# Kernel optimization log

Hardware: AMD Instinct MI355X
Metric: run time of the kernel (lower is better)

The kernel has to match this reference:

```python
import jax, jax.numpy as jnp
import numpy as np

NUM_HEADS = 16
PAD_ID = 0.0  # max(config.pad_id, 0)


def setup_inputs() -> dict:
    key = jax.random.key(0)
    ks = jax.random.split(key, 9)
    B, T, C = 2, 2048, 1024
    x = jax.random.normal(ks[0], (B, T, C), dtype=jnp.float32)
    # xavier_uniform-like scale for square [C, C] weights
    lim = (6.0 / (C + C)) ** 0.5
    def w(k):
        return jax.random.uniform(k, (C, C), dtype=jnp.float32, minval=-lim, maxval=lim)
    def b(k):
        return jax.random.uniform(k, (C,), dtype=jnp.float32)  # nn.init.uniform_ default [0,1)
    return {
        "x": x,
        "wq_w": w(ks[1]), "wq_b": b(ks[2]),
        "wk_w": w(ks[3]), "wk_b": b(ks[4]),
        "wv_w": w(ks[5]), "wv_b": b(ks[6]),
        "wo_w": w(ks[7]), "wo_b": b(ks[8]),
    }


def reference(x, wq_w, wq_b, wk_w, wk_b, wv_w, wv_b, wo_w, wo_b):
    B, T, C = x.shape
    H = NUM_HEADS
    Dh = C // H
    scale = Dh ** -0.5

    # Linear layers (torch Linear: x @ W.T + b), then split heads -> [B, T, H, Dh]
    q = (x @ wq_w.T + wq_b).reshape(B, T, H, Dh)
    k = (x @ wk_w.T + wk_b).reshape(B, T, H, Dh)
    v = (x @ wv_w.T + wv_b).reshape(B, T, H, Dh)

    # scores: [B, H, Tq, Tk]
    scores = jnp.einsum("bthd,bshd->bhts", q, k) * scale

    # Padding mask over keys: (x[:,:,0] != pad_id) -> [B, 1, 1, Tk]
    key_mask = (x[:, :, 0] != PAD_ID)[:, None, None, :]
    scores = jnp.where(key_mask, scores, -jnp.inf)

    attn = jax.nn.softmax(scores, axis=-1)

    out = jnp.einsum("bhts,bshd->bthd", attn, v).reshape(B, T, C)
    return out @ wo_w.T + wo_b
```

## Files before the change

### kernel.cpp

```cpp
#include <hip/hip_runtime.h>
#include <hip/hip_bf16.h>

typedef short short8 __attribute__((ext_vector_type(8)));
typedef float f32x4 __attribute__((ext_vector_type(4)));

#define MFMA32(a, b, c) __builtin_amdgcn_mfma_f32_16x16x32_bf16(a, b, c, 0, 0, 0)

#if __has_builtin(__builtin_amdgcn_exp2f)
#define EXP2F(x) __builtin_amdgcn_exp2f(x)
#else
#define EXP2F(x) exp2f(x)
#endif

#define GLL16(gp, lp) __builtin_amdgcn_global_load_lds(                                  \
    (__attribute__((address_space(1))) unsigned int*)(unsigned long long)(const void*)(gp), \
    (__attribute__((address_space(3))) unsigned int*)(lp), 16, 0, 0)

__device__ __forceinline__ unsigned short f2b(float f) {
    union { float f; unsigned int u; } v;
    v.f = f;
    unsigned int u = v.u;
    return (unsigned short)((u + 0x7fffu + ((u >> 16) & 1u)) >> 16);
}

static __device__ __forceinline__ f32x4 max4(f32x4 x, f32x4 y) {
    f32x4 r;
    r[0] = fmaxf(x[0], y[0]); r[1] = fmaxf(x[1], y[1]);
    r[2] = fmaxf(x[2], y[2]); r[3] = fmaxf(x[3], y[3]);
    return r;
}

__global__ void cvt_all(const float* __restrict__ x,
                        const float* __restrict__ w0, const float* __restrict__ w1,
                        const float* __restrict__ w2, const float* __restrict__ w3,
                        unsigned short* __restrict__ xb, unsigned short* __restrict__ wb,
                        float* __restrict__ maskbuf) {
    int blk = blockIdx.x;
    if (blk < 4096) {
        int i = blk * 256 + threadIdx.x;
        float4 v = ((const float4*)x)[i];
        ushort4 o;
        o.x = f2b(v.x); o.y = f2b(v.y); o.z = f2b(v.z); o.w = f2b(v.w);
        ((ushort4*)xb)[i] = o;
        if ((i & 255) == 0)
            maskbuf[i >> 8] = (v.x != 0.0f) ? 0.0f : -1e30f;
    } else {
        int wi = blk - 4096;
        int widx = wi >> 10;
        int i = (wi & 1023) * 256 + threadIdx.x;
        const float* src = widx == 0 ? w0 : (widx == 1 ? w1 : (widx == 2 ? w2 : w3));
        float4 v = ((const float4*)src)[i];
        ushort4 o;
        o.x = f2b(v.x); o.y = f2b(v.y); o.z = f2b(v.z); o.w = f2b(v.w);
        ((ushort4*)(wb + ((size_t)widx << 20)))[i] = o;
    }
}

#define QSCALE (0.125f * 1.44269504088896341f)

__global__ __launch_bounds__(256) void gemm_qkv(
        const unsigned short* __restrict__ A,
        const unsigned short* __restrict__ wq, const unsigned short* __restrict__ wk,
        const unsigned short* __restrict__ wv,
        const float* __restrict__ bq, const float* __restrict__ bk,
        const float* __restrict__ bv,
        unsigned short* __restrict__ qbuf, unsigned short* __restrict__ kbuf,
        unsigned short* __restrict__ vbuf) {
    __shared__ __attribute__((aligned(16))) unsigned short As[2][128 * 32];
    __shared__ __attribute__((aligned(16))) unsigned short Bs[2][128 * 32];
    int tid = threadIdx.x;
    int lane = tid & 63, wave = tid >> 6;
    int lane15 = lane & 15, quad = lane >> 4;
    int seg = blockIdx.x >> 3;
    int bn = (blockIdx.x & 7) * 128;
    int bm = blockIdx.y * 128;
    const unsigned short* Bw = seg == 0 ? wq : (seg == 1 ? wk : wv);
    const float* bias = seg == 0 ? bq : (seg == 1 ? bk : bv);
    int wm = (wave >> 1) * 64, wn = (wave & 1) * 64;

    f32x4 acc[4][4];
#pragma unroll
    for (int i = 0; i < 4; i++)
#pragma unroll
        for (int j = 0; j < 4; j++) acc[i][j] = (f32x4){0.f, 0.f, 0.f, 0.f};

    int arow = tid >> 2, acol = (tid & 3) * 8;
    const unsigned short* A0 = &A[(size_t)(bm + arow) * 1024 + acol];
    const unsigned short* A1 = A0 + (size_t)64 * 1024;
    const unsigned short* B0 = &Bw[(size_t)(bn + arow) * 1024 + acol];
    const unsigned short* B1 = B0 + (size_t)64 * 1024;

    GLL16(A0, &As[0][(size_t)tid * 8]);
    GLL16(A1, &As[0][(size_t)(tid + 256) * 8]);
    GLL16(B0, &Bs[0][(size_t)tid * 8]);
    GLL16(B1, &Bs[0][(size_t)(tid + 256) * 8]);

    for (int it = 0; it < 32; it++) {
        int cur = it & 1;
        __syncthreads();
        if (it < 31) {
            int kn = (it + 1) * 32;
            GLL16(A0 + kn, &As[cur ^ 1][(size_t)tid * 8]);
            GLL16(A1 + kn, &As[cur ^ 1][(size_t)(tid + 256) * 8]);
            GLL16(B0 + kn, &Bs[cur ^ 1][(size_t)tid * 8]);
            GLL16(B1 + kn, &Bs[cur ^ 1][(size_t)(tid + 256) * 8]);
        }
        const unsigned short* as = As[cur];
        const unsigned short* bs = Bs[cur];
        short8 af[4], bf[4];
#pragma unroll
        for (int i = 0; i < 4; i++)
            af[i] = *(const short8*)&as[(wm + i * 16 + lane15) * 32 + quad * 8];
#pragma unroll
        for (int j = 0; j < 4; j++)
            bf[j] = *(const short8*)&bs[(wn + j * 16 + lane15) * 32 + quad * 8];
#pragma unroll
        for (int i = 0; i < 4; i++)
#pragma unroll
            for (int j = 0; j < 4; j++)
                acc[i][j] = MFMA32(af[i], bf[j], acc[i][j]);
    }

    int bb = bm >> 11;
#pragma unroll
    for (int j = 0; j < 4; j++) {
        int nl = bn + wn + j * 16 + lane15;
        int h = nl >> 6, d = nl & 63;
        float bv_ = bias[nl];
        if (seg == 2) {
            size_t vbase = ((size_t)((bb * 16 + h) * 64 + d)) * 2048;
#pragma unroll
            for (int i = 0; i < 4; i++) {
                int tk0 = (bm & 2047) + wm + i * 16 + quad * 4;
                int grp = tk0 >> 5;
                ushort4 pk;
                pk.x = f2b(acc[i][j][0] + bv_);
                pk.y = f2b(acc[i][j][1] + bv_);
                pk.z = f2b(acc[i][j][2] + bv_);
                pk.w = f2b(acc[i][j][3] + bv_);
                *(ushort4*)&vbuf[vbase + grp * 32 + quad * 8 + (i & 1) * 4] = pk;
            }
        } else {
#pragma unroll
            for (int i = 0; i < 4; i++)
#pragma unroll
                for (int r = 0; r < 4; r++) {
                    int m = bm + wm + i * 16 + quad * 4 + r;
                    int tk = m & 2047;
                    float v = acc[i][j][r] + bv_;
                    size_t off = ((size_t)((bb * 16 + h) * 2048 + tk)) * 64 + d;
                    if (seg == 0) qbuf[off] = f2b(v * QSCALE);
                    else          kbuf[off] = f2b(v);
                }
        }
    }
}

__global__ __launch_bounds__(256) void gemm_proj(
        const unsigned short* __restrict__ A, const unsigned short* __restrict__ Bw,
        const float* __restrict__ bias, float* __restrict__ out) {
    __shared__ __attribute__((aligned(16))) unsigned short As[2][64 * 32];
    __shared__ __attribute__((aligned(16))) unsigned short Bs[2][128 * 32];
    int tid = threadIdx.x;
    int lane = tid & 63, wave = tid >> 6;
    int lane15 = lane & 15, quad = lane >> 4;
    int bn = blockIdx.x * 128, bm = blockIdx.y * 64;
    int wm = (wave >> 1) * 32, wn = (wave & 1) * 64;

    f32x4 acc[2][4];
#pragma unroll
    for (int i = 0; i < 2; i++)
#pragma unroll
        for (int j = 0; j < 4; j++) acc[i][j] = (f32x4){0.f, 0.f, 0.f, 0.f};

    int arow = tid >> 2, acol = (tid & 3) * 8;
    const unsigned short* A0 = &A[(size_t)(bm + arow) * 1024 + acol];
    const unsigned short* B0 = &Bw[(size_t)(bn + arow) * 1024 + acol];
    const unsigned short* B1 = B0 + (size_t)64 * 1024;

    GLL16(A0, &As[0][(size_t)tid * 8]);
    GLL16(B0, &Bs[0][(size_t)tid * 8]);
    GLL16(B1, &Bs[0][(size_t)(tid + 256) * 8]);

    for (int it = 0; it < 32; it++) {
        int cur = it & 1;
        __syncthreads();
        if (it < 31) {
            int kn = (it + 1) * 32;
            GLL16(A0 + kn, &As[cur ^ 1][(size_t)tid * 8]);
            GLL16(B0 + kn, &Bs[cur ^ 1][(size_t)tid * 8]);
            GLL16(B1 + kn, &Bs[cur ^ 1][(size_t)(tid + 256) * 8]);
        }
        const unsigned short* as = As[cur];
        const unsigned short* bs = Bs[cur];
        short8 af[2], bf[4];
#pragma unroll
        for (int i = 0; i < 2; i++)
            af[i] = *(const short8*)&as[(wm + i * 16 + lane15) * 32 + quad * 8];
#pragma unroll
        for (int j = 0; j < 4; j++)
            bf[j] = *(const short8*)&bs[(wn + j * 16 + lane15) * 32 + quad * 8];
#pragma unroll
        for (int i = 0; i < 2; i++)
#pragma unroll
            for (int j = 0; j < 4; j++)
                acc[i][j] = MFMA32(af[i], bf[j], acc[i][j]);
    }

#pragma unroll
    for (int j = 0; j < 4; j++) {
        int n = bn + wn + j * 16 + lane15;
        float bv_ = bias[n];
#pragma unroll
        for (int i = 0; i < 2; i++)
#pragma unroll
            for (int r = 0; r < 4; r++) {
                int m = bm + wm + i * 16 + quad * 4 + r;
                out[(size_t)m * 1024 + n] = acc[i][j][r] + bv_;
            }
    }
}

__global__ __launch_bounds__(256, 2) void attn_kernel(
        const unsigned short* __restrict__ qbuf, const unsigned short* __restrict__ kbuf,
        const unsigned short* __restrict__ vtbuf, const float* __restrict__ maskbuf,
        unsigned short* __restrict__ attnout) {
    __shared__ __attribute__((aligned(16))) unsigned short Ks[2][128 * 64];
    __shared__ __attribute__((aligned(16))) unsigned short Vs[2][64 * 128];

    int id = blockIdx.x;
    int combo = (id & 7) | (((id >> 7) & 3) << 3);
    int qt = (id >> 3) & 15;
    int b = combo >> 4, h = combo & 15;
    int tid = threadIdx.x, lane = tid & 63, wave = tid >> 6;
    int lane15 = lane & 15, quad = lane >> 4;
    int q0 = qt * 128 + wave * 32;

    const unsigned short* Q  = qbuf  + (size_t)combo * 2048 * 64;
    const unsigned short* Kp = kbuf  + (size_t)combo * 2048 * 64;
    const unsigned short* Vt = vtbuf + (size_t)combo * 64 * 2048;
    const float* mb = maskbuf + b * 2048;

    short8 qf[2][2];
#pragma unroll
    for (int a = 0; a < 2; a++)
#pragma unroll
        for (int g = 0; g < 2; g++)
            qf[a][g] = *(const short8*)&Q[(size_t)(q0 + a * 16 + lane15) * 64 + g * 32 + quad * 8];

    int ci0 = tid;
    float m_run[2] = {-1e30f, -1e30f}, l_run[2] = {0.f, 0.f};
    f32x4 o[2][4];
#pragma unroll
    for (int a = 0; a < 2; a++)
#pragma unroll
        for (int c = 0; c < 4; c++) o[a][c] = (f32x4){0.f, 0.f, 0.f, 0.f};

    const f32x4 z4 = {0.f, 0.f, 0.f, 0.f};
    int x7 = lane15 & 7;

#pragma unroll
    for (int r4 = 0; r4 < 4; r4++) {
        int ci = ci0 + r4 * 256;
        int kr = ci >> 3, kc = (ci & 7) ^ (kr & 7);
        GLL16(&Kp[(size_t)kr * 64 + kc * 8], &Ks[0][(size_t)ci * 8]);
        int vd = ci >> 4, vc = (ci & 15) ^ (vd & 15);
        GLL16(&Vt[(size_t)vd * 2048 + vc * 8], &Vs[0][(size_t)ci * 8]);
    }

    for (int it = 0; it < 16; it++) {
        int cur = it & 1;
        int kb = it * 128;
        __syncthreads();
        if (it < 15) {
            int kn = kb + 128;
#pragma unroll
            for (int r4 = 0; r4 < 4; r4++) {
                int ci = ci0 + r4 * 256;
                int kr = ci >> 3, kc = (ci & 7) ^ (kr & 7);
                GLL16(&Kp[(size_t)(kn + kr) * 64 + kc * 8], &Ks[cur ^ 1][(size_t)ci * 8]);
                int vd = ci >> 4, vc = (ci & 15) ^ (vd & 15);
                GLL16(&Vt[(size_t)vd * 2048 + kn + vc * 8], &Vs[cur ^ 1][(size_t)ci * 8]);
            }
        }
        const unsigned short* ks = Ks[cur];
        const unsigned short* vs = Vs[cur];

        f32x4 s[2][8];
#pragma unroll
        for (int t = 0; t < 8; t++) {
            int row = t * 16 + lane15;
            short8 k0 = *(const short8*)&ks[row * 64 + (quad ^ x7) * 8];
            short8 k1 = *(const short8*)&ks[row * 64 + ((quad + 4) ^ x7) * 8];
            f32x4 t0 = MFMA32(k0, qf[0][0], z4);
            s[0][t] = MFMA32(k1, qf[0][1], t0);
            f32x4 t1 = MFMA32(k0, qf[1][0], z4);
            s[1][t] = MFMA32(k1, qf[1][1], t1);
        }
#pragma unroll
        for (int t = 0; t < 8; t++) {
            f32x4 mkt = *(const f32x4*)&mb[kb + t * 16 + quad * 4];
            s[0][t] += mkt;
            s[1][t] += mkt;
        }
        short8 pb8[2][4];
#pragma unroll
        for (int a = 0; a < 2; a++) {
            f32x4 m4 = s[a][0];
#pragma unroll
            for (int t = 1; t < 8; t++) m4 = max4(m4, s[a][t]);
            float mx = fmaxf(fmaxf(m4[0], m4[1]), fmaxf(m4[2], m4[3]));
            mx = fmaxf(mx, __shfl_xor(mx, 16));
            mx = fmaxf(mx, __shfl_xor(mx, 32));
            float mnew = fmaxf(m_run[a], mx);
            float alpha = EXP2F(m_run[a] - mnew);
            m_run[a] = mnew;
            float ls = 0.f;
#pragma unroll
            for (int g = 0; g < 4; g++) {
                float e0 = EXP2F(s[a][2 * g][0] - mnew);
                float e1 = EXP2F(s[a][2 * g][1] - mnew);
                float e2 = EXP2F(s[a][2 * g][2] - mnew);
                float e3 = EXP2F(s[a][2 * g][3] - mnew);
                float f0 = EXP2F(s[a][2 * g + 1][0] - mnew);
                float f1 = EXP2F(s[a][2 * g + 1][1] - mnew);
                float f2 = EXP2F(s[a][2 * g + 1][2] - mnew);
                float f3 = EXP2F(s[a][2 * g + 1][3] - mnew);
                ls += ((e0 + e1) + (e2 + e3)) + ((f0 + f1) + (f2 + f3));
                union { uint4 u; short8 sv; } pu;
                pu.u.x = __builtin_amdgcn_perm(__float_as_uint(e1), __float_as_uint(e0), 0x07060302u);
                pu.u.y = __builtin_amdgcn_perm(__float_as_uint(e3), __float_as_uint(e2), 0x07060302u);
                pu.u.z = __builtin_amdgcn_perm(__float_as_uint(f1), __float_as_uint(f0), 0x07060302u);
                pu.u.w = __builtin_amdgcn_perm(__float_as_uint(f3), __float_as_uint(f2), 0x07060302u);
                pb8[a][g] = pu.sv;
            }
            l_run[a] = l_run[a] * alpha + ls;
#pragma unroll
            for (int c = 0; c < 4; c++) o[a][c] *= alpha;
        }
#pragma unroll
        for (int c = 0; c < 4; c++) {
            int d = c * 16 + lane15;
#pragma unroll
            for (int g = 0; g < 4; g++) {
                int skc = (g * 4 + quad) ^ lane15;
                short8 vv = *(const short8*)&vs[d * 128 + skc * 8];
                o[0][c] = MFMA32(vv, pb8[0][g], o[0][c]);
                o[1][c] = MFMA32(vv, pb8[1][g], o[1][c]);
            }
        }
    }

#pragma unroll
    for (int a = 0; a < 2; a++) {
        float l = l_run[a];
        l += __shfl_xor(l, 16);
        l += __shfl_xor(l, 32);
        float rl = 1.0f / l;
        size_t row = (size_t)(b * 2048 + q0 + a * 16 + lane15) * 1024 + h * 64 + quad * 4;
#pragma unroll
        for (int c = 0; c < 4; c++) {
            ushort4 pk;
            pk.x = f2b(o[a][c][0] * rl);
            pk.y = f2b(o[a][c][1] * rl);
            pk.z = f2b(o[a][c][2] * rl);
            pk.w = f2b(o[a][c][3] * rl);
            *(ushort4*)&attnout[row + c * 16] = pk;
        }
    }
}

extern "C" void kernel_launch(void* const* d_in, const int* in_sizes, int n_in,
                              void* d_out, int out_size, void* d_ws, size_t ws_size,
                              hipStream_t stream) {
    const float* x    = (const float*)d_in[0];
    const float* wq_w = (const float*)d_in[1];
    const float* wq_b = (const float*)d_in[2];
    const float* wk_w = (const float*)d_in[3];
    const float* wk_b = (const float*)d_in[4];
    const float* wv_w = (const float*)d_in[5];
    const float* wv_b = (const float*)d_in[6];
    const float* wo_w = (const float*)d_in[7];
    const float* wo_b = (const float*)d_in[8];
    float* out = (float*)d_out;

    char* ws = (char*)d_ws;
    size_t off = 0;
    unsigned short* xb      = (unsigned short*)(ws + off); off += (size_t)4096 * 1024 * 2;
    unsigned short* wb      = (unsigned short*)(ws + off); off += (size_t)4 * 1024 * 1024 * 2;
    unsigned short* qbuf    = (unsigned short*)(ws + off); off += (size_t)4096 * 1024 * 2;
    unsigned short* kbuf    = (unsigned short*)(ws + off); off += (size_t)4096 * 1024 * 2;
    unsigned short* vbuf    = (unsigned short*)(ws + off); off += (size_t)4096 * 1024 * 2;
    unsigned short* attnout = (unsigned short*)(ws + off); off += (size_t)4096 * 1024 * 2;
    float* maskbuf          = (float*)(ws + off);          off += 4096 * 4;

    unsigned short* wqb = wb;
    unsigned short* wkb = wb + (1u << 20);
    unsigned short* wvb = wb + (2u << 20);
    unsigned short* wob = wb + (3u << 20);

    cvt_all<<<8192, 256, 0, stream>>>(x, wq_w, wk_w, wv_w, wo_w, xb, wb, maskbuf);

    gemm_qkv<<<dim3(24, 32), 256, 0, stream>>>(xb, wqb, wkb, wvb,
                                               wq_b, wk_b, wv_b, qbuf, kbuf, vbuf);

    attn_kernel<<<512, 256, 0, stream>>>(qbuf, kbuf, vbuf, maskbuf, attnout);

    gemm_proj<<<dim3(8, 64), 256, 0, stream>>>(attnout, wob, wo_b, out);
}
```

Before: 218.5 us.

## Load K/V fragments directly from global into registers, dropping LDS double buffer

The attention kernel no longer stages K and V tiles through double-buffered shared memory with global_load_lds and __syncthreads. Each wave now loads its own K and V MFMA fragments straight from global memory into registers, prefetching V while the softmax runs. It also raises wave priority around the MFMA sections with s_setprio. This removes block-level barriers and LDS traffic, but every wave in the block re-reads the same K/V tiles from global/L2 instead of sharing them, and register pressure rises.

```diff
diff --git a/kernel.cpp b/kernel.cpp
--- a/kernel.cpp
+++ b/kernel.cpp
@@ -225,9 +225,6 @@
         const unsigned short* __restrict__ qbuf, const unsigned short* __restrict__ kbuf,
         const unsigned short* __restrict__ vtbuf, const float* __restrict__ maskbuf,
         unsigned short* __restrict__ attnout) {
-    __shared__ __attribute__((aligned(16))) unsigned short Ks[2][128 * 64];
-    __shared__ __attribute__((aligned(16))) unsigned short Vs[2][64 * 128];
-
     int id = blockIdx.x;
     int combo = (id & 7) | (((id >> 7) & 3) << 3);
     int qt = (id >> 3) & 15;
@@ -248,7 +245,6 @@
         for (int g = 0; g < 2; g++)
             qf[a][g] = *(const short8*)&Q[(size_t)(q0 + a * 16 + lane15) * 64 + g * 32 + quad * 8];
 
-    int ci0 = tid;
     float m_run[2] = {-1e30f, -1e30f}, l_run[2] = {0.f, 0.f};
     f32x4 o[2][4];
 #pragma unroll
@@ -257,52 +253,46 @@
         for (int c = 0; c < 4; c++) o[a][c] = (f32x4){0.f, 0.f, 0.f, 0.f};
 
     const f32x4 z4 = {0.f, 0.f, 0.f, 0.f};
-    int x7 = lane15 & 7;
-
-#pragma unroll
-    for (int r4 = 0; r4 < 4; r4++) {
-        int ci = ci0 + r4 * 256;
-        int kr = ci >> 3, kc = (ci & 7) ^ (kr & 7);
-        GLL16(&Kp[(size_t)kr * 64 + kc * 8], &Ks[0][(size_t)ci * 8]);
-        int vd = ci >> 4, vc = (ci & 15) ^ (vd & 15);
-        GLL16(&Vt[(size_t)vd * 2048 + vc * 8], &Vs[0][(size_t)ci * 8]);
-    }
+
+    const unsigned short* Krow = &Kp[(size_t)lane15 * 64 + quad * 8];
+    const unsigned short* Vrow = &Vt[(size_t)lane15 * 2048 + quad * 8];
 
     for (int it = 0; it < 16; it++) {
-        int cur = it & 1;
         int kb = it * 128;
-        __syncthreads();
-        if (it < 15) {
-            int kn = kb + 128;
-#pragma unroll
-            for (int r4 = 0; r4 < 4; r4++) {
-                int ci = ci0 + r4 * 256;
-                int kr = ci >> 3, kc = (ci & 7) ^ (kr & 7);
-                GLL16(&Kp[(size_t)(kn + kr) * 64 + kc * 8], &Ks[cur ^ 1][(size_t)ci * 8]);
-                int vd = ci >> 4, vc = (ci & 15) ^ (vd & 15);
-                GLL16(&Vt[(size_t)vd * 2048 + kn + vc * 8], &Vs[cur ^ 1][(size_t)ci * 8]);
-            }
-        }
-        const unsigned short* ks = Ks[cur];
-        const unsigned short* vs = Vs[cur];
+
+        short8 k0[8], k1[8];
+#pragma unroll
+        for (int t = 0; t < 8; t++) {
+            const unsigned short* kr = Krow + (size_t)(kb + t * 16) * 64;
+            k0[t] = *(const short8*)kr;
+            k1[t] = *(const short8*)(kr + 32);
+        }
 
         f32x4 s[2][8];
+        __builtin_amdgcn_s_setprio(1);
 #pragma unroll
         for (int t = 0; t < 8; t++) {
-            int row = t * 16 + lane15;
-            short8 k0 = *(const short8*)&ks[row * 64 + (quad ^ x7) * 8];
-            short8 k1 = *(const short8*)&ks[row * 64 + ((quad + 4) ^ x7) * 8];
-            f32x4 t0 = MFMA32(k0, qf[0][0], z4);
-            s[0][t] = MFMA32(k1, qf[0][1], t0);
-            f32x4 t1 = MFMA32(k0, qf[1][0], z4);
-            s[1][t] = MFMA32(k1, qf[1][1], t1);
-        }
+            f32x4 t0 = MFMA32(k0[t], qf[0][0], z4);
+            s[0][t] = MFMA32(k1[t], qf[0][1], t0);
+            f32x4 t1 = MFMA32(k0[t], qf[1][0], z4);
+            s[1][t] = MFMA32(k1[t], qf[1][1], t1);
+        }
+        __builtin_amdgcn_s_setprio(0);
+
+        short8 vf[4][4];
+#pragma unroll
+        for (int c = 0; c < 4; c++)
+#pragma unroll
+            for (int g = 0; g < 4; g++)
+                vf[c][g] = *(const short8*)(Vrow + (size_t)c * 16 * 2048 + kb + g * 32);
+
 #pragma unroll
         for (int t = 0; t < 8; t++) {
             f32x4 mkt = *(const f32x4*)&mb[kb + t * 16 + quad * 4];
             s[0][t] += mkt;
             s[1][t] += mkt;
         }
+
         short8 pb8[2][4];
 #pragma unroll
         for (int a = 0; a < 2; a++) {
@@ -338,17 +328,16 @@
 #pragma unroll
             for (int c = 0; c < 4; c++) o[a][c] *= alpha;
         }
-#pragma unroll
-        for (int c = 0; c < 4; c++) {
-            int d = c * 16 + lane15;
+
+        __builtin_amdgcn_s_setprio(1);
+#pragma unroll
+        for (int c = 0; c < 4; c++)
 #pragma unroll
             for (int g = 0; g < 4; g++) {
-                int skc = (g * 4 + quad) ^ lane15;
-                short8 vv = *(const short8*)&vs[d * 128 + skc * 8];
-                o[0][c] = MFMA32(vv, pb8[0][g], o[0][c]);
-                o[1][c] = MFMA32(vv, pb8[1][g], o[1][c]);
+                o[0][c] = MFMA32(vf[c][g], pb8[0][g], o[0][c]);
+                o[1][c] = MFMA32(vf[c][g], pb8[1][g], o[1][c]);
             }
-        }
+        __builtin_amdgcn_s_setprio(0);
     }
 
 #pragma unroll
```

Measured after the change: 273.1 us. 25.0% more time.

## Split attention block into 8 waves of 16 query rows each

Applied to the files above, without the earlier changes.

The attention kernel now launches 512 threads per block, and each of the 8 waves handles 16 query rows instead of 32. This halves per-wave register state (Q fragments, score tiles, accumulators), allows more waves per CU via launch bounds (512,4), and spreads the K/V tile load across more threads. In exchange, every K and V fragment read from LDS now feeds only one MFMA instead of two, so LDS traffic per FLOP doubles and there is less instruction-level parallelism per wave.

```diff
diff --git a/kernel.cpp b/kernel.cpp
--- a/kernel.cpp
+++ b/kernel.cpp
@@ -221,7 +221,7 @@
     }
 }
 
-__global__ __launch_bounds__(256, 2) void attn_kernel(
+__global__ __launch_bounds__(512, 4) void attn_kernel(
         const unsigned short* __restrict__ qbuf, const unsigned short* __restrict__ kbuf,
         const unsigned short* __restrict__ vtbuf, const float* __restrict__ maskbuf,
         unsigned short* __restrict__ attnout) {
@@ -234,34 +234,30 @@
     int b = combo >> 4, h = combo & 15;
     int tid = threadIdx.x, lane = tid & 63, wave = tid >> 6;
     int lane15 = lane & 15, quad = lane >> 4;
-    int q0 = qt * 128 + wave * 32;
+    int q0 = qt * 128 + wave * 16;
 
     const unsigned short* Q  = qbuf  + (size_t)combo * 2048 * 64;
     const unsigned short* Kp = kbuf  + (size_t)combo * 2048 * 64;
     const unsigned short* Vt = vtbuf + (size_t)combo * 64 * 2048;
     const float* mb = maskbuf + b * 2048;
 
-    short8 qf[2][2];
-#pragma unroll
-    for (int a = 0; a < 2; a++)
-#pragma unroll
-        for (int g = 0; g < 2; g++)
-            qf[a][g] = *(const short8*)&Q[(size_t)(q0 + a * 16 + lane15) * 64 + g * 32 + quad * 8];
-
-    int ci0 = tid;
-    float m_run[2] = {-1e30f, -1e30f}, l_run[2] = {0.f, 0.f};
-    f32x4 o[2][4];
-#pragma unroll
-    for (int a = 0; a < 2; a++)
-#pragma unroll
-        for (int c = 0; c < 4; c++) o[a][c] = (f32x4){0.f, 0.f, 0.f, 0.f};
+    short8 qf[2];
+#pragma unroll
+    for (int g = 0; g < 2; g++)
+        qf[g] = *(const short8*)&Q[(size_t)(q0 + lane15) * 64 + g * 32 + quad * 8];
+
+    float m_run = -1e30f, l_run = 0.f;
+    f32x4 o[4];
+#pragma unroll
+    for (int c = 0; c < 4; c++) o[c] = (f32x4){0.f, 0.f, 0.f, 0.f};
 
     const f32x4 z4 = {0.f, 0.f, 0.f, 0.f};
     int x7 = lane15 & 7;
-
-#pragma unroll
-    for (int r4 = 0; r4 < 4; r4++) {
-        int ci = ci0 + r4 * 256;
+    int ci0 = tid;
+
+#pragma unroll
+    for (int r2 = 0; r2 < 2; r2++) {
+        int ci = ci0 + r2 * 512;
         int kr = ci >> 3, kc = (ci & 7) ^ (kr & 7);
         GLL16(&Kp[(size_t)kr * 64 + kc * 8], &Ks[0][(size_t)ci * 8]);
         int vd = ci >> 4, vc = (ci & 15) ^ (vd & 15);
@@ -275,8 +271,8 @@
         if (it < 15) {
             int kn = kb + 128;
 #pragma unroll
-            for (int r4 = 0; r4 < 4; r4++) {
-                int ci = ci0 + r4 * 256;
+            for (int r2 = 0; r2 < 2; r2++) {
+                int ci = ci0 + r2 * 512;
                 int kr = ci >> 3, kc = (ci & 7) ^ (kr & 7);
                 GLL16(&Kp[(size_t)(kn + kr) * 64 + kc * 8], &Ks[cur ^ 1][(size_t)ci * 8]);
                 int vd = ci >> 4, vc = (ci & 15) ^ (vd & 15);
@@ -286,58 +282,52 @@
         const unsigned short* ks = Ks[cur];
         const unsigned short* vs = Vs[cur];
 
-        f32x4 s[2][8];
+        f32x4 s[8];
 #pragma unroll
         for (int t = 0; t < 8; t++) {
             int row = t * 16 + lane15;
             short8 k0 = *(const short8*)&ks[row * 64 + (quad ^ x7) * 8];
             short8 k1 = *(const short8*)&ks[row * 64 + ((quad + 4) ^ x7) * 8];
-            f32x4 t0 = MFMA32(k0, qf[0][0], z4);
-            s[0][t] = MFMA32(k1, qf[0][1], t0);
-            f32x4 t1 = MFMA32(k0, qf[1][0], z4);
-            s[1][t] = MFMA32(k1, qf[1][1], t1);
-        }
-#pragma unroll
-        for (int t = 0; t < 8; t++) {
-            f32x4 mkt = *(const f32x4*)&mb[kb + t * 16 + quad * 4];
-            s[0][t] += mkt;
-            s[1][t] += mkt;
-        }
-        short8 pb8[2][4];
-#pragma unroll
-        for (int a = 0; a < 2; a++) {
-            f32x4 m4 = s[a][0];
-#pragma unroll
-            for (int t = 1; t < 8; t++) m4 = max4(m4, s[a][t]);
-            float mx = fmaxf(fmaxf(m4[0], m4[1]), fmaxf(m4[2], m4[3]));
-            mx = fmaxf(mx, __shfl_xor(mx, 16));
-            mx = fmaxf(mx, __shfl_xor(mx, 32));
-            float mnew = fmaxf(m_run[a], mx);
-            float alpha = EXP2F(m_run[a] - mnew);
-            m_run[a] = mnew;
-            float ls = 0.f;
-#pragma unroll
-            for (int g = 0; g < 4; g++) {
-                float e0 = EXP2F(s[a][2 * g][0] - mnew);
-                float e1 = EXP2F(s[a][2 * g][1] - mnew);
-                float e2 = EXP2F(s[a][2 * g][2] - mnew);
-                float e3 = EXP2F(s[a][2 * g][3] - mnew);
-                float f0 = EXP2F(s[a][2 * g + 1][0] - mnew);
-                float f1 = EXP2F(s[a][2 * g + 1][1] - mnew);
-                float f2 = EXP2F(s[a][2 * g + 1][2] - mnew);
-                float f3 = EXP2F(s[a][2 * g + 1][3] - mnew);
-                ls += ((e0 + e1) + (e2 + e3)) + ((f0 + f1) + (f2 + f3));
-                union { uint4 u; short8 sv; } pu;
-                pu.u.x = __builtin_amdgcn_perm(__float_as_uint(e1), __float_as_uint(e0), 0x07060302u);
-                pu.u.y = __builtin_amdgcn_perm(__float_as_uint(e3), __float_as_uint(e2), 0x07060302u);
-                pu.u.z = __builtin_amdgcn_perm(__float_as_uint(f1), __float_as_uint(f0), 0x07060302u);
-                pu.u.w = __builtin_amdgcn_perm(__float_as_uint(f3), __float_as_uint(f2), 0x07060302u);
-                pb8[a][g] = pu.sv;
-            }
-            l_run[a] = l_run[a] * alpha + ls;
-#pragma unroll
-            for (int c = 0; c < 4; c++) o[a][c] *= alpha;
-        }
+            f32x4 t0 = MFMA32(k0, qf[0], z4);
+            s[t] = MFMA32(k1, qf[1], t0);
+        }
+#pragma unroll
+        for (int t = 0; t < 8; t++)
+            s[t] += *(const f32x4*)&mb[kb + t * 16 + quad * 4];
+
+        f32x4 m4 = s[0];
+#pragma unroll
+        for (int t = 1; t < 8; t++) m4 = max4(m4, s[t]);
+        float mx = fmaxf(fmaxf(m4[0], m4[1]), fmaxf(m4[2], m4[3]));
+        mx = fmaxf(mx, __shfl_xor(mx, 16));
+        mx = fmaxf(mx, __shfl_xor(mx, 32));
+        float mnew = fmaxf(m_run, mx);
+        float alpha = EXP2F(m_run - mnew);
+        m_run = mnew;
+        float ls = 0.f;
+        short8 pb8[4];
+#pragma unroll
+        for (int g = 0; g < 4; g++) {
+            float e0 = EXP2F(s[2 * g][0] - mnew);
+            float e1 = EXP2F(s[2 * g][1] - mnew);
+            float e2 = EXP2F(s[2 * g][2] - mnew);
+            float e3 = EXP2F(s[2 * g][3] - mnew);
+            float f0 = EXP2F(s[2 * g + 1][0] - mnew);
+            float f1 = EXP2F(s[2 * g + 1][1] - mnew);
+            float f2 = EXP2F(s[2 * g + 1][2] - mnew);
+            float f3 = EXP2F(s[2 * g + 1][3] - mnew);
+            ls += ((e0 + e1) + (e2 + e3)) + ((f0 + f1) + (f2 + f3));
+            union { uint4 u; short8 sv; } pu;
+            pu.u.x = __builtin_amdgcn_perm(__float_as_uint(e1), __float_as_uint(e0), 0x07060302u);
+            pu.u.y = __builtin_amdgcn_perm(__float_as_uint(e3), __float_as_uint(e2), 0x07060302u);
+            pu.u.z = __builtin_amdgcn_perm(__float_as_uint(f1), __float_as_uint(f0), 0x07060302u);
+            pu.u.w = __builtin_amdgcn_perm(__float_as_uint(f3), __float_as_uint(f2), 0x07060302u);
+            pb8[g] = pu.sv;
+        }
+        l_run = l_run * alpha + ls;
+#pragma unroll
+        for (int c = 0; c < 4; c++) o[c] *= alpha;
+
 #pragma unroll
         for (int c = 0; c < 4; c++) {
             int d = c * 16 + lane15;
@@ -345,28 +335,24 @@
             for (int g = 0; g < 4; g++) {
                 int skc = (g * 4 + quad) ^ lane15;
                 short8 vv = *(const short8*)&vs[d * 128 + skc * 8];
-                o[0][c] = MFMA32(vv, pb8[0][g], o[0][c]);
-                o[1][c] = MFMA32(vv, pb8[1][g], o[1][c]);
+                o[c] = MFMA32(vv, pb8[g], o[c]);
             }
         }
     }
 
-#pragma unroll
-    for (int a = 0; a < 2; a++) {
-        float l = l_run[a];
-        l += __shfl_xor(l, 16);
-        l += __shfl_xor(l, 32);
-        float rl = 1.0f / l;
-        size_t row = (size_t)(b * 2048 + q0 + a * 16 + lane15) * 1024 + h * 64 + quad * 4;
-#pragma unroll
-        for (int c = 0; c < 4; c++) {
-            ushort4 pk;
-            pk.x = f2b(o[a][c][0] * rl);
-            pk.y = f2b(o[a][c][1] * rl);
-            pk.z = f2b(o[a][c][2] * rl);
-            pk.w = f2b(o[a][c][3] * rl);
-            *(ushort4*)&attnout[row + c * 16] = pk;
-        }
+    float l = l_run;
+    l += __shfl_xor(l, 16);
+    l += __shfl_xor(l, 32);
+    float rl = 1.0f / l;
+    size_t row = (size_t)(b * 2048 + q0 + lane15) * 1024 + h * 64 + quad * 4;
+#pragma unroll
+    for (int c = 0; c < 4; c++) {
+        ushort4 pk;
+        pk.x = f2b(o[c][0] * rl);
+        pk.y = f2b(o[c][1] * rl);
+        pk.z = f2b(o[c][2] * rl);
+        pk.w = f2b(o[c][3] * rl);
+        *(ushort4*)&attnout[row + c * 16] = pk;
     }
 }
 
@@ -404,7 +390,7 @@
     gemm_qkv<<<dim3(24, 32), 256, 0, stream>>>(xb, wqb, wkb, wvb,
                                                wq_b, wk_b, wv_b, qbuf, kbuf, vbuf);
 
-    attn_kernel<<<512, 256, 0, stream>>>(qbuf, kbuf, vbuf, maskbuf, attnout);
+    attn_kernel<<<512, 512, 0, stream>>>(qbuf, kbuf, vbuf, maskbuf, attnout);
 
     gemm_proj<<<dim3(8, 64), 256, 0, stream>>>(attnout, wob, wo_b, out);
 }
```

Result: faster. 213.7 us (-2.2%).
